# Kernel optimization log

Hardware: AMD Instinct MI355X
Metric: run time of the kernel (lower is better)

Reference implementation:

```python
import jax, jax.numpy as jnp
import numpy as np

B, T, C, HS = 256, 256, 384, 64


def setup_inputs() -> dict:
    key = jax.random.key(0)
    k1, k2, k3, k4 = jax.random.split(key, 4)
    X = jax.random.normal(k1, (B, T, C), dtype=jnp.float32)
    Wq = jax.random.normal(k2, (C, HS), dtype=jnp.float32) * (C ** -0.5)
    Wk = jax.random.normal(k3, (C, HS), dtype=jnp.float32) * (C ** -0.5)
    Wv = jax.random.normal(k4, (C, HS), dtype=jnp.float32) * (C ** -0.5)
    return {"X": X, "Wq": Wq, "Wk": Wk, "Wv": Wv}


def reference(X, Wq, Wk, Wv):
    # Single causal self-attention head (dropout in eval mode / identity).
    num_channels = X.shape[-1]
    q = jnp.einsum('btc,ch->bth', X, Wq)  # [B,T,HS]
    k = jnp.einsum('btc,ch->bth', X, Wk)
    v = jnp.einsum('btc,ch->bth', X, Wv)
    # NOTE: original scales by embedding dim C**-0.5, not head_size**-0.5.
    scores = jnp.einsum('bqh,bkh->bqk', q, k) * (num_channels ** -0.5)  # [B,T,T]
    Tq = X.shape[1]
    causal = jnp.tril(jnp.ones((Tq, Tq), dtype=bool))
    scores = jnp.where(causal, scores, jnp.float32(-jnp.inf))
    weights = jax.nn.softmax(scores, axis=-1)
    return jnp.einsum('bqk,bkh->bqh', weights, v)  # [B,T,HS]
```

## Files before the change

kernel.cpp:

```cpp
#include <hip/hip_runtime.h>
#include <hip/hip_bf16.h>

#define B_  256
#define T_  256
#define C_  384
#define HS_ 64
#define BT_ (B_*T_)

typedef __attribute__((ext_vector_type(8))) short short8;
typedef __attribute__((ext_vector_type(4))) float f32x4;

__device__ __forceinline__ unsigned short f2bf(float f) {
    unsigned u = __float_as_uint(f);
    u += 0x7FFFu + ((u >> 16) & 1u);
    return (unsigned short)(u >> 16);
}

__global__ __launch_bounds__(256) void prep_wfrag(
    const float* __restrict__ Wq, const float* __restrict__ Wk,
    const float* __restrict__ Wv, unsigned short* __restrict__ Wfrag)
{
    const int tid  = blockIdx.x * 256 + threadIdx.x;
    const int lane = tid & 63;
    const int q    = tid >> 6;
    const int f    = q % 3;
    const int q2   = q / 3;
    const int wn   = q2 & 3;
    const int s    = q2 >> 2;

    const int n     = wn * 48 + f * 16 + (lane & 15);
    const int kbase = s * 32 + (lane >> 4) * 8;
    const float* src = (n < 64) ? Wq : (n < 128) ? Wk : Wv;
    const int c      = n & 63;
    const float scale = (n < 64) ? 0.05103103630798288f : 1.0f;

    short8 out;
    #pragma unroll
    for (int j = 0; j < 8; ++j)
        out[j] = (short)f2bf(src[(size_t)(kbase + j) * HS_ + c] * scale);
    *(short8*)&Wfrag[(size_t)tid * 8] = out;
}

#define LQ_OFF 0
#define LK_OFF 18432
#define LV_OFF 36864
#define LX_OFF 53760
#define LDSP   40

__global__ __launch_bounds__(1024, 4) void head_fused(
    const float* __restrict__ X, const unsigned short* __restrict__ Wfrag,
    float* __restrict__ out)
{
    __shared__ unsigned short lds[74240];
    const int t    = threadIdx.x;
    const int w    = t >> 6;
    const int lane = t & 63;
    const int lo   = lane & 15;
    const int hi   = lane >> 4;
    const int b    = blockIdx.x;
    const int wm   = w >> 2, wn = w & 3;

    const float* Xb = X + (size_t)b * T_ * C_;
    const short8* Wf = (const short8*)Wfrag;

    const int srow  = t >> 2;
    const int squad = t & 3;

    auto stage_load = [&](int k0, float4* g) {
        const float* p = Xb + (size_t)srow * C_ + k0 + squad * 8;
        g[0] = *(const float4*)(p);
        g[1] = *(const float4*)(p + 4);
    };
    auto stage_write = [&](int buf, const float4* g) {
        short8 p;
        p[0] = (short)f2bf(g[0].x); p[1] = (short)f2bf(g[0].y);
        p[2] = (short)f2bf(g[0].z); p[3] = (short)f2bf(g[0].w);
        p[4] = (short)f2bf(g[1].x); p[5] = (short)f2bf(g[1].y);
        p[6] = (short)f2bf(g[1].z); p[7] = (short)f2bf(g[1].w);
        *(short8*)&lds[LX_OFF + buf * 10240 + srow * 40 + squad * 8] = p;
    };
    auto load_w = [&](int s, short8* wf) {
        const short8* base = Wf + ((size_t)(s * 4 + wn) * 3) * 64 + lane;
        #pragma unroll
        for (int f = 0; f < 3; ++f)
            wf[f] = base[f * 64];
    };

    float4 gx[2][2];
    short8 wfr[2][3];
    stage_load(0, gx[0]);
    load_w(0, wfr[0]);
    stage_load(32, gx[1]);
    stage_write(0, gx[0]);
    __syncthreads();

    f32x4 acc[4][3];
    #pragma unroll
    for (int m = 0; m < 4; ++m)
        #pragma unroll
        for (int f = 0; f < 3; ++f)
            acc[m][f] = (f32x4){0.f, 0.f, 0.f, 0.f};

    #pragma unroll 2
    for (int s = 0; s < 12; ++s) {
        const int cur = s & 1;
        if (s < 10) stage_load((s + 2) * 32, gx[cur]);
        if (s < 11) load_w(s + 1, wfr[cur ^ 1]);
        if (s < 11) stage_write(cur ^ 1, gx[cur ^ 1]);

        short8 af[4];
        #pragma unroll
        for (int m = 0; m < 4; ++m)
            af[m] = *(const short8*)&lds[LX_OFF + cur * 10240 + (wm * 64 + m * 16 + lo) * 40 + hi * 8];
        #pragma unroll
        for (int m = 0; m < 4; ++m)
            #pragma unroll
            for (int f = 0; f < 3; ++f)
                acc[m][f] = __builtin_amdgcn_mfma_f32_16x16x32_bf16(af[m], wfr[cur][f], acc[m][f], 0, 0, 0);
        __syncthreads();
    }

    #pragma unroll
    for (int m = 0; m < 4; ++m) {
        const int rowb = wm * 64 + m * 16 + hi * 4;
        #pragma unroll
        for (int f = 0; f < 3; ++f) {
            const int base = wn * 48 + f * 16;
            if (base < 64) {
                #pragma unroll
                for (int r = 0; r < 4; ++r)
                    lds[LQ_OFF + (rowb + r) * 72 + base + lo] = f2bf(acc[m][f][r]);
            } else if (base < 128) {
                #pragma unroll
                for (int r = 0; r < 4; ++r)
                    lds[LK_OFF + (rowb + r) * 72 + (base - 64) + lo] = f2bf(acc[m][f][r]);
            } else {
                ushort4 pk = { f2bf(acc[m][f][0]), f2bf(acc[m][f][1]),
                               f2bf(acc[m][f][2]), f2bf(acc[m][f][3]) };
                *(ushort4*)&lds[LV_OFF + (base - 128 + lo) * 264 + rowb] = pk;
            }
        }
    }
    __syncthreads();

    unsigned short* Pw = &lds[LX_OFF + w * 640];

    const int sg  = w & 3, pos = w >> 2;
    const int tq  = (pos == 0) ? sg : (pos == 1) ? 15 - sg : (pos == 2) ? 4 + sg : 11 - sg;

    {
        const int q_lane = tq * 16 + lo;
        short8 qf0 = *(const short8*)&lds[LQ_OFF + q_lane * 72 + hi * 8];
        short8 qf1 = *(const short8*)&lds[LQ_OFF + q_lane * 72 + hi * 8 + 32];

        f32x4 acc_o[4];
        #pragma unroll
        for (int n = 0; n < 4; ++n) acc_o[n] = (f32x4){0.f, 0.f, 0.f, 0.f};
        float Mr = -1e30f, Lr = 0.f;

        const int nsteps = (tq >> 1) + 1;
        for (int s = 0; s < nsteps; ++s) {
            const int kv0 = s * 32;
            f32x4 sb[2];
            sb[0] = (f32x4){0.f, 0.f, 0.f, 0.f};
            sb[1] = (f32x4){0.f, 0.f, 0.f, 0.f};
            __builtin_amdgcn_s_setprio(1);
            #pragma unroll
            for (int n = 0; n < 2; ++n) {
                const unsigned short* kb = &lds[LK_OFF + (kv0 + n * 16 + lo) * 72 + hi * 8];
                short8 kf0 = *(const short8*)kb;
                short8 kf1 = *(const short8*)(kb + 32);
                sb[n] = __builtin_amdgcn_mfma_f32_16x16x32_bf16(kf0, qf0, sb[n], 0, 0, 0);
                sb[n] = __builtin_amdgcn_mfma_f32_16x16x32_bf16(kf1, qf1, sb[n], 0, 0, 0);
            }
            __builtin_amdgcn_s_setprio(0);
            if (s == nsteps - 1) {
                #pragma unroll
                for (int n = 0; n < 2; ++n)
                    #pragma unroll
                    for (int r = 0; r < 4; ++r)
                        if (kv0 + n * 16 + hi * 4 + r > q_lane) sb[n][r] = -1e30f;
            }
            float pmax = fmaxf(fmaxf(fmaxf(sb[0][0], sb[0][1]), fmaxf(sb[0][2], sb[0][3])),
                               fmaxf(fmaxf(sb[1][0], sb[1][1]), fmaxf(sb[1][2], sb[1][3])));
            pmax = fmaxf(pmax, __shfl_xor(pmax, 16));
            pmax = fmaxf(pmax, __shfl_xor(pmax, 32));
            float Mn;
            if (__all(pmax - Mr <= 8.0f)) {
                Mn = Mr;
            } else {
                Mn = fmaxf(Mr, pmax);
                const float fr = __expf(Mr - Mn);
                Mr = Mn;
                Lr *= fr;
                #pragma unroll
                for (int n = 0; n < 4; ++n) {
                    acc_o[n][0] *= fr; acc_o[n][1] *= fr;
                    acc_o[n][2] *= fr; acc_o[n][3] *= fr;
                }
            }
            float p0 = __expf(sb[0][0] - Mn), p1 = __expf(sb[0][1] - Mn);
            float p2 = __expf(sb[0][2] - Mn), p3 = __expf(sb[0][3] - Mn);
            float p4 = __expf(sb[1][0] - Mn), p5 = __expf(sb[1][1] - Mn);
            float p6 = __expf(sb[1][2] - Mn), p7 = __expf(sb[1][3] - Mn);
            float ls = ((p0 + p1) + (p2 + p3)) + ((p4 + p5) + (p6 + p7));
            ls += __shfl_xor(ls, 16);
            ls += __shfl_xor(ls, 32);
            Lr += ls;
            ushort4 w0 = { f2bf(p0), f2bf(p1), f2bf(p2), f2bf(p3) };
            ushort4 w1 = { f2bf(p4), f2bf(p5), f2bf(p6), f2bf(p7) };
            *(ushort4*)&Pw[lo * LDSP + hi * 4]      = w0;
            *(ushort4*)&Pw[lo * LDSP + 16 + hi * 4] = w1;
            short8 pf = *(const short8*)&Pw[lo * LDSP + hi * 8];
            __builtin_amdgcn_s_setprio(1);
            #pragma unroll
            for (int n = 0; n < 4; ++n) {
                short8 vf = *(const short8*)&lds[LV_OFF + (n * 16 + lo) * 264 + kv0 + hi * 8];
                acc_o[n] = __builtin_amdgcn_mfma_f32_16x16x32_bf16(vf, pf, acc_o[n], 0, 0, 0);
            }
            __builtin_amdgcn_s_setprio(0);
        }
        const float inv = 1.0f / Lr;
        float* op = out + ((size_t)(b * 256 + q_lane)) * HS_;
        #pragma unroll
        for (int n = 0; n < 4; ++n)
            #pragma unroll
            for (int r = 0; r < 4; ++r)
                op[n * 16 + hi * 4 + r] = acc_o[n][r] * inv;
    }
}

extern "C" void kernel_launch(void* const* d_in, const int* in_sizes, int n_in,
                              void* d_out, int out_size, void* d_ws, size_t ws_size,
                              hipStream_t stream) {
    const float* X  = (const float*)d_in[0];
    const float* Wq = (const float*)d_in[1];
    const float* Wk = (const float*)d_in[2];
    const float* Wv = (const float*)d_in[3];
    float* out = (float*)d_out;

    unsigned short* Wfrag = (unsigned short*)d_ws;

    prep_wfrag<<<36, 256, 0, stream>>>(Wq, Wk, Wv, Wfrag);
    head_fused<<<B_, 1024, 0, stream>>>(X, Wfrag, out);
}
```

Before: 36.04 us.

## Split fused attention kernel into separate QKV projection and attention kernels

Splits the single fused kernel, one block per batch element, into two kernels. The first computes the Q/K/V projection with 64-row, 256-thread blocks (1024 blocks) and writes bf16 Q, K and transposed V to workspace. The second loads K and V into LDS and runs the causal attention. This raises parallelism and occupancy in the projection phase and shrinks LDS use per attention block. The cost is an extra launch and a global-memory round trip for Q, K and V.

```diff
diff --git a/kernel.cpp b/kernel.cpp
--- a/kernel.cpp
+++ b/kernel.cpp
@@ -41,26 +41,20 @@
     *(short8*)&Wfrag[(size_t)tid * 8] = out;
 }
 
-#define LQ_OFF 0
-#define LK_OFF 18432
-#define LV_OFF 36864
-#define LX_OFF 53760
-#define LDSP   40
-
-__global__ __launch_bounds__(1024, 4) void head_fused(
+__global__ __launch_bounds__(256, 4) void qkv_a(
     const float* __restrict__ X, const unsigned short* __restrict__ Wfrag,
-    float* __restrict__ out)
+    unsigned short* __restrict__ Qg, unsigned short* __restrict__ Kg,
+    unsigned short* __restrict__ Vtg)
 {
-    __shared__ unsigned short lds[74240];
+    __shared__ unsigned short Xs[2][64 * 40];
     const int t    = threadIdx.x;
     const int w    = t >> 6;
     const int lane = t & 63;
     const int lo   = lane & 15;
     const int hi   = lane >> 4;
-    const int b    = blockIdx.x;
-    const int wm   = w >> 2, wn = w & 3;
-
-    const float* Xb = X + (size_t)b * T_ * C_;
+    const int row0 = blockIdx.x * 64;
+
+    const float* Xb = X + (size_t)row0 * C_;
     const short8* Wf = (const short8*)Wfrag;
 
     const int srow  = t >> 2;
@@ -77,10 +71,10 @@
         p[2] = (short)f2bf(g[0].z); p[3] = (short)f2bf(g[0].w);
         p[4] = (short)f2bf(g[1].x); p[5] = (short)f2bf(g[1].y);
         p[6] = (short)f2bf(g[1].z); p[7] = (short)f2bf(g[1].w);
-        *(short8*)&lds[LX_OFF + buf * 10240 + srow * 40 + squad * 8] = p;
+        *(short8*)&Xs[buf][srow * 40 + squad * 8] = p;
     };
     auto load_w = [&](int s, short8* wf) {
-        const short8* base = Wf + ((size_t)(s * 4 + wn) * 3) * 64 + lane;
+        const short8* base = Wf + ((size_t)(s * 4 + w) * 3) * 64 + lane;
         #pragma unroll
         for (int f = 0; f < 3; ++f)
             wf[f] = base[f * 64];
@@ -111,7 +105,7 @@
         short8 af[4];
         #pragma unroll
         for (int m = 0; m < 4; ++m)
-            af[m] = *(const short8*)&lds[LX_OFF + cur * 10240 + (wm * 64 + m * 16 + lo) * 40 + hi * 8];
+            af[m] = *(const short8*)&Xs[cur][(m * 16 + lo) * 40 + hi * 8];
         #pragma unroll
         for (int m = 0; m < 4; ++m)
             #pragma unroll
@@ -122,36 +116,75 @@
 
     #pragma unroll
     for (int m = 0; m < 4; ++m) {
-        const int rowb = wm * 64 + m * 16 + hi * 4;
+        const int grow = row0 + m * 16 + hi * 4;
         #pragma unroll
         for (int f = 0; f < 3; ++f) {
-            const int base = wn * 48 + f * 16;
+            const int base = w * 48 + f * 16;
+            const int n    = base + lo;
             if (base < 64) {
                 #pragma unroll
                 for (int r = 0; r < 4; ++r)
-                    lds[LQ_OFF + (rowb + r) * 72 + base + lo] = f2bf(acc[m][f][r]);
+                    Qg[(size_t)(grow + r) * HS_ + n] = f2bf(acc[m][f][r]);
             } else if (base < 128) {
                 #pragma unroll
                 for (int r = 0; r < 4; ++r)
-                    lds[LK_OFF + (rowb + r) * 72 + (base - 64) + lo] = f2bf(acc[m][f][r]);
+                    Kg[(size_t)(grow + r) * HS_ + (n - 64)] = f2bf(acc[m][f][r]);
             } else {
                 ushort4 pk = { f2bf(acc[m][f][0]), f2bf(acc[m][f][1]),
                                f2bf(acc[m][f][2]), f2bf(acc[m][f][3]) };
-                *(ushort4*)&lds[LV_OFF + (base - 128 + lo) * 264 + rowb] = pk;
-            }
+                *(ushort4*)&Vtg[((size_t)(grow >> 8) * 64 + (n - 128)) * 256 + (grow & 255)] = pk;
+            }
+        }
+    }
+}
+
+#define BK_OFF 0
+#define BV_OFF 18432
+#define BP_OFF 35328
+#define LDSP   40
+
+__global__ __launch_bounds__(1024, 4) void attn_b(
+    const unsigned short* __restrict__ Qg,
+    const unsigned short* __restrict__ Kg,
+    const unsigned short* __restrict__ Vtg,
+    float* __restrict__ out)
+{
+    __shared__ unsigned short lds[45568];
+    const int t    = threadIdx.x;
+    const int w    = t >> 6;
+    const int lane = t & 63;
+    const int lo   = lane & 15;
+    const int hi   = lane >> 4;
+    const int b    = blockIdx.x;
+
+    {
+        const uint4* gk = (const uint4*)(Kg + (size_t)b * 256 * HS_);
+        #pragma unroll
+        for (int i = 0; i < 2; ++i) {
+            int idx = t + i * 1024;
+            int r = idx >> 3, c8 = (idx & 7) * 8;
+            *(uint4*)&lds[BK_OFF + r * 72 + c8] = gk[idx];
+        }
+        const uint4* gv = (const uint4*)(Vtg + (size_t)b * 64 * 256);
+        #pragma unroll
+        for (int i = 0; i < 2; ++i) {
+            int idx = t + i * 1024;
+            int r = idx >> 5, c8 = (idx & 31) * 8;
+            *(uint4*)&lds[BV_OFF + r * 264 + c8] = gv[idx];
         }
     }
     __syncthreads();
 
-    unsigned short* Pw = &lds[LX_OFF + w * 640];
+    unsigned short* Pw = &lds[BP_OFF + w * 640];
 
     const int sg  = w & 3, pos = w >> 2;
     const int tq  = (pos == 0) ? sg : (pos == 1) ? 15 - sg : (pos == 2) ? 4 + sg : 11 - sg;
 
     {
         const int q_lane = tq * 16 + lo;
-        short8 qf0 = *(const short8*)&lds[LQ_OFF + q_lane * 72 + hi * 8];
-        short8 qf1 = *(const short8*)&lds[LQ_OFF + q_lane * 72 + hi * 8 + 32];
+        const unsigned short* qp = Qg + ((size_t)(b * 256 + q_lane)) * HS_ + hi * 8;
+        short8 qf0 = *(const short8*)qp;
+        short8 qf1 = *(const short8*)(qp + 32);
 
         f32x4 acc_o[4];
         #pragma unroll
@@ -167,7 +200,7 @@
             __builtin_amdgcn_s_setprio(1);
             #pragma unroll
             for (int n = 0; n < 2; ++n) {
-                const unsigned short* kb = &lds[LK_OFF + (kv0 + n * 16 + lo) * 72 + hi * 8];
+                const unsigned short* kb = &lds[BK_OFF + (kv0 + n * 16 + lo) * 72 + hi * 8];
                 short8 kf0 = *(const short8*)kb;
                 short8 kf1 = *(const short8*)(kb + 32);
                 sb[n] = __builtin_amdgcn_mfma_f32_16x16x32_bf16(kf0, qf0, sb[n], 0, 0, 0);
@@ -215,7 +248,7 @@
             __builtin_amdgcn_s_setprio(1);
             #pragma unroll
             for (int n = 0; n < 4; ++n) {
-                short8 vf = *(const short8*)&lds[LV_OFF + (n * 16 + lo) * 264 + kv0 + hi * 8];
+                short8 vf = *(const short8*)&lds[BV_OFF + (n * 16 + lo) * 264 + kv0 + hi * 8];
                 acc_o[n] = __builtin_amdgcn_mfma_f32_16x16x32_bf16(vf, pf, acc_o[n], 0, 0, 0);
             }
             __builtin_amdgcn_s_setprio(0);
@@ -240,7 +273,11 @@
     float* out = (float*)d_out;
 
     unsigned short* Wfrag = (unsigned short*)d_ws;
+    unsigned short* Qg    = Wfrag + (size_t)9216 * 8;
+    unsigned short* Kg    = Qg + (size_t)BT_ * HS_;
+    unsigned short* Vtg   = Kg + (size_t)BT_ * HS_;
 
     prep_wfrag<<<36, 256, 0, stream>>>(Wq, Wk, Wv, Wfrag);
-    head_fused<<<B_, 1024, 0, stream>>>(X, Wfrag, out);
-}
+    qkv_a<<<BT_ / 64, 256, 0, stream>>>(X, Wfrag, Qg, Kg, Vtg);
+    attn_b<<<B_, 1024, 0, stream>>>(Qg, Kg, Vtg, out);
+}
```

Result: slower. 42.99 us (+19.3%).
